# Performance work log

Hardware: AMD Instinct MI355X
Metric: run time of the kernel (lower is better)

Reference implementation:

```python
import jax, jax.numpy as jnp
import numpy as np

N_POINTS = 8192
N_DIM = 2
N_PAIRS = 262144


def setup_inputs() -> dict:
    key = jax.random.key(0)
    k1, k2, k3, k4 = jax.random.split(key, 4)
    logits = jax.random.normal(k1, (N_POINTS, N_DIM), dtype=jnp.float32)
    i = jax.random.randint(k2, (N_PAIRS,), 0, N_POINTS, dtype=jnp.int64)
    j = jax.random.randint(k3, (N_PAIRS,), 0, N_POINTS, dtype=jnp.int64)
    pij = jax.random.uniform(k4, (N_PAIRS,), dtype=jnp.float32, minval=1e-6, maxval=1.0)
    pij = pij / jnp.sum(pij)  # joint probabilities, strictly positive
    return {"pij": pij, "i": i, "j": j, "logits": logits}


def reference(pij, i, j, logits):
    # Pairwise squared distances via the norm expansion (same math as the
    # N x N x D expanded-subtract in the torch original, without the huge tensor).
    sq = jnp.sum(logits * logits, axis=1)                      # [N]
    dkl2 = sq[:, None] + sq[None, :] - 2.0 * (logits @ logits.T)  # [N, N]
    n_diag = logits.shape[0]
    # Student-t partition function, excluding the diagonal (each diag term is 1).
    part = jnp.sum(1.0 / (1.0 + dkl2)) - n_diag
    xi = logits[i]                                              # [E, D]
    xj = logits[j]                                              # [E, D]
    # NOTE: torch adds 1.0 elementwise BEFORE summing over D, so this is
    # (D + ||xi-xj||^2)^-1 — reproduced faithfully.
    num = 1.0 / jnp.sum(1.0 + (xi - xj) ** 2, axis=1)           # [E]
    qij = num / part
    return jnp.sum(pij * (jnp.log(pij) - jnp.log(qij)))
```

## Files before the change

### kernel.cpp

```cpp
#include <hip/hip_runtime.h>
#include <math.h>

#define N_POINTS 8192
#define N_PAIRS  262144

constexpr int BLOCKS  = 512;
constexpr int THREADS = 256;
constexpr int TILE    = 8;
constexpr int NTILES  = N_POINTS / TILE;
constexpr int EPB     = N_PAIRS / BLOCKS;

typedef float f32x2 __attribute__((ext_vector_type(2)));

__global__ __launch_bounds__(THREADS)
void fused_kernel(const float* __restrict__ logits,
                  const float* __restrict__ pij,
                  const int* __restrict__ ei,
                  const int* __restrict__ ej,
                  float* __restrict__ partials) {
    __shared__ float2 pts[N_POINTS];
    __shared__ float wred[3][THREADS / 64];

    const int t = threadIdx.x;
    const int b = blockIdx.x;

    {
        const float4* src = (const float4*)logits;
        float4* dst = (float4*)pts;
        #pragma unroll
        for (int k = t; k < N_POINTS / 2; k += THREADS) dst[k] = src[k];
    }

    const int2   ea = ((const int2*)(ei + b * EPB))[t];
    const int2   eb = ((const int2*)(ej + b * EPB))[t];
    const float2 pp = ((const float2*)(pij + b * EPB))[t];

    __syncthreads();

    const int v1 = b;
    const int v2 = NTILES - 1 - b;

    auto sweep = [&](int v) -> float {
        const int r0 = v * TILE;
        f32x2 rxv[TILE], ryv[TILE], acc[TILE];
        #pragma unroll
        for (int r = 0; r < TILE; ++r) {
            const float2 pr = pts[r0 + r];
            rxv[r] = (f32x2){pr.x, pr.x};
            ryv[r] = (f32x2){pr.y, pr.y};
            acc[r] = (f32x2){0.0f, 0.0f};
        }
        #pragma unroll 2
        for (int k = r0 + 2 * t; k < N_POINTS; k += 2 * THREADS) {
            const float4 qq = *(const float4*)&pts[k];
            const f32x2 qx = (f32x2){qq.x, qq.z};
            const f32x2 qy = (f32x2){qq.y, qq.w};
            #pragma unroll
            for (int r = 0; r < TILE; ++r) {
                const f32x2 dx = rxv[r] - qx;
                const f32x2 dy = ryv[r] - qy;
                const f32x2 d2 = dx * dx + dy * dy + 1.0f;
                acc[r] += (f32x2){__builtin_amdgcn_rcpf(d2.x),
                                  __builtin_amdgcn_rcpf(d2.y)};
            }
        }
        float s = 0.0f;
        #pragma unroll
        for (int r = 0; r < TILE; ++r) s += acc[r].x + acc[r].y;
        return s;
    };

    float T = sweep(v1) + sweep(v2);

    float Dc = 0.0f;
    if (t < 128) {
        const int v = (t < 64) ? v1 : v2;
        const int l = t & 63;
        const int i = v * TILE + (l >> 3);
        const int k = v * TILE + (l & 7);
        const float dx = pts[i].x - pts[k].x;
        const float dy = pts[i].y - pts[k].y;
        const float d2 = __builtin_fmaf(dx, dx, __builtin_fmaf(dy, dy, 1.0f));
        Dc = __builtin_amdgcn_rcpf(d2);
    }
    float part = __builtin_fmaf(2.0f, T, -Dc);

    float s1 = 0.0f, sp = 0.0f;
    {
        float2 pa = pts[ea.x], pb = pts[eb.x];
        float dx = pa.x - pb.x, dy = pa.y - pb.y;
        float d2 = __builtin_fmaf(dx, dx, __builtin_fmaf(dy, dy, 2.0f));
        s1 += pp.x * (__logf(pp.x) + __logf(d2));
        sp += pp.x;

        pa = pts[ea.y]; pb = pts[eb.y];
        dx = pa.x - pb.x; dy = pa.y - pb.y;
        d2 = __builtin_fmaf(dx, dx, __builtin_fmaf(dy, dy, 2.0f));
        s1 += pp.y * (__logf(pp.y) + __logf(d2));
        sp += pp.y;
    }

    #pragma unroll
    for (int off = 32; off > 0; off >>= 1) {
        part += __shfl_down(part, off, 64);
        s1   += __shfl_down(s1,   off, 64);
        sp   += __shfl_down(sp,   off, 64);
    }
    const int w = t >> 6, l = t & 63;
    if (l == 0) { wred[0][w] = part; wred[1][w] = s1; wred[2][w] = sp; }
    __syncthreads();
    if (t == 0) {
        float r0s = 0.f, r1s = 0.f, r2s = 0.f;
        #pragma unroll
        for (int i = 0; i < THREADS / 64; ++i) {
            r0s += wred[0][i]; r1s += wred[1][i]; r2s += wred[2][i];
        }
        partials[0 * BLOCKS + b] = r0s;
        partials[1 * BLOCKS + b] = r1s;
        partials[2 * BLOCKS + b] = r2s;
    }
}

__global__ __launch_bounds__(256)
void final_kernel(const float* __restrict__ partials, float* __restrict__ out) {
    __shared__ double ra[4], rs[4], rp[4];
    const int t = threadIdx.x;

    double a = (double)partials[0 * BLOCKS + t] + (double)partials[0 * BLOCKS + t + 256];
    double s = (double)partials[1 * BLOCKS + t] + (double)partials[1 * BLOCKS + t + 256];
    double p = (double)partials[2 * BLOCKS + t] + (double)partials[2 * BLOCKS + t + 256];

    #pragma unroll
    for (int off = 32; off > 0; off >>= 1) {
        a += __shfl_down(a, off, 64);
        s += __shfl_down(s, off, 64);
        p += __shfl_down(p, off, 64);
    }
    const int w = t >> 6, l = t & 63;
    if (l == 0) { ra[w] = a; rs[w] = s; rp[w] = p; }
    __syncthreads();
    if (t == 0) {
        double A = 0.0, S = 0.0, P = 0.0;
        #pragma unroll
        for (int i = 0; i < 4; ++i) { A += ra[i]; S += rs[i]; P += rp[i]; }
        A -= (double)N_POINTS;
        out[0] = (float)(S + log(A) * P);
    }
}

extern "C" void kernel_launch(void* const* d_in, const int* in_sizes, int n_in,
                              void* d_out, int out_size, void* d_ws, size_t ws_size,
                              hipStream_t stream) {
    const float* pij    = (const float*)d_in[0];
    const int*   ei     = (const int*)d_in[1];
    const int*   ej     = (const int*)d_in[2];
    const float* logits = (const float*)d_in[3];
    float* out = (float*)d_out;

    float* partials = (float*)d_ws;

    fused_kernel<<<BLOCKS, THREADS, 0, stream>>>(logits, pij, ei, ej, partials);
    final_kernel<<<1, 256, 0, stream>>>(partials, out);
}
```

Before: 73.16 us.

## Read points directly from global memory and double block count with smaller tiles

Drops the per-block staging of all 8192 points into 64KB of shared memory and reads point coordinates straight from global memory through the cache, including the random gathers for pair indices. The grid doubles to 1024 blocks with 4-row tiles so each thread handles one pair, and the sweep loop unroll goes up to 4. This removes the large per-block LDS fill and its barrier and relieves the LDS limit on occupancy. In exchange the inner loop now issues global/L2 loads instead of LDS reads, and each block does less reuse per loaded point.

```diff
diff --git a/kernel.cpp b/kernel.cpp
--- a/kernel.cpp
+++ b/kernel.cpp
@@ -4,9 +4,9 @@
 #define N_POINTS 8192
 #define N_PAIRS  262144
 
-constexpr int BLOCKS  = 512;
+constexpr int BLOCKS  = 1024;
 constexpr int THREADS = 256;
-constexpr int TILE    = 8;
+constexpr int TILE    = 4;
 constexpr int NTILES  = N_POINTS / TILE;
 constexpr int EPB     = N_PAIRS / BLOCKS;
 
@@ -18,24 +18,16 @@
                   const int* __restrict__ ei,
                   const int* __restrict__ ej,
                   float* __restrict__ partials) {
-    __shared__ float2 pts[N_POINTS];
     __shared__ float wred[3][THREADS / 64];
 
     const int t = threadIdx.x;
     const int b = blockIdx.x;
 
-    {
-        const float4* src = (const float4*)logits;
-        float4* dst = (float4*)pts;
-        #pragma unroll
-        for (int k = t; k < N_POINTS / 2; k += THREADS) dst[k] = src[k];
-    }
+    const int   ia = ei[b * EPB + t];
+    const int   ja = ej[b * EPB + t];
+    const float pp = pij[b * EPB + t];
 
-    const int2   ea = ((const int2*)(ei + b * EPB))[t];
-    const int2   eb = ((const int2*)(ej + b * EPB))[t];
-    const float2 pp = ((const float2*)(pij + b * EPB))[t];
-
-    __syncthreads();
+    const float2* __restrict__ pts = (const float2*)logits;
 
     const int v1 = b;
     const int v2 = NTILES - 1 - b;
@@ -50,7 +42,7 @@
             ryv[r] = (f32x2){pr.y, pr.y};
             acc[r] = (f32x2){0.0f, 0.0f};
         }
-        #pragma unroll 2
+        #pragma unroll 4
         for (int k = r0 + 2 * t; k < N_POINTS; k += 2 * THREADS) {
             const float4 qq = *(const float4*)&pts[k];
             const f32x2 qx = (f32x2){qq.x, qq.z};
@@ -73,11 +65,11 @@
     float T = sweep(v1) + sweep(v2);
 
     float Dc = 0.0f;
-    if (t < 128) {
-        const int v = (t < 64) ? v1 : v2;
-        const int l = t & 63;
-        const int i = v * TILE + (l >> 3);
-        const int k = v * TILE + (l & 7);
+    if (t < 2 * TILE * TILE) {
+        const int v = (t < TILE * TILE) ? v1 : v2;
+        const int l = t & (TILE * TILE - 1);
+        const int i = v * TILE + (l >> 2);
+        const int k = v * TILE + (l & 3);
         const float dx = pts[i].x - pts[k].x;
         const float dy = pts[i].y - pts[k].y;
         const float d2 = __builtin_fmaf(dx, dx, __builtin_fmaf(dy, dy, 1.0f));
@@ -85,19 +77,13 @@
     }
     float part = __builtin_fmaf(2.0f, T, -Dc);
 
-    float s1 = 0.0f, sp = 0.0f;
+    float s1, sp;
     {
-        float2 pa = pts[ea.x], pb = pts[eb.x];
-        float dx = pa.x - pb.x, dy = pa.y - pb.y;
-        float d2 = __builtin_fmaf(dx, dx, __builtin_fmaf(dy, dy, 2.0f));
-        s1 += pp.x * (__logf(pp.x) + __logf(d2));
-        sp += pp.x;
-
-        pa = pts[ea.y]; pb = pts[eb.y];
-        dx = pa.x - pb.x; dy = pa.y - pb.y;
-        d2 = __builtin_fmaf(dx, dx, __builtin_fmaf(dy, dy, 2.0f));
-        s1 += pp.y * (__logf(pp.y) + __logf(d2));
-        sp += pp.y;
+        const float2 pa = pts[ia], pb = pts[ja];
+        const float dx = pa.x - pb.x, dy = pa.y - pb.y;
+        const float d2 = __builtin_fmaf(dx, dx, __builtin_fmaf(dy, dy, 2.0f));
+        s1 = pp * (__logf(pp) + __logf(d2));
+        sp = pp;
     }
 
     #pragma unroll
@@ -126,9 +112,13 @@
     __shared__ double ra[4], rs[4], rp[4];
     const int t = threadIdx.x;
 
-    double a = (double)partials[0 * BLOCKS + t] + (double)partials[0 * BLOCKS + t + 256];
-    double s = (double)partials[1 * BLOCKS + t] + (double)partials[1 * BLOCKS + t + 256];
-    double p = (double)partials[2 * BLOCKS + t] + (double)partials[2 * BLOCKS + t + 256];
+    double a = 0.0, s = 0.0, p = 0.0;
+    #pragma unroll
+    for (int q = 0; q < BLOCKS / 256; ++q) {
+        a += (double)partials[0 * BLOCKS + t + 256 * q];
+        s += (double)partials[1 * BLOCKS + t + 256 * q];
+        p += (double)partials[2 * BLOCKS + t + 256 * q];
+    }
 
     #pragma unroll
     for (int off = 32; off > 0; off >>= 1) {
```

Result: faster. 71.48 us (-2.3%).
